# Performance work log

Measured on AMD Instinct MI355X. Metric: run time of the kernel, lower is better.

## Reference

```python
import jax, jax.numpy as jnp
import numpy as np

B, A, C = 64, 8732, 81


def setup_inputs() -> dict:
    key = jax.random.key(0)
    k1, k2, k3, k4, k5 = jax.random.split(key, 5)
    scores = jax.random.normal(k1, (B, A, C), dtype=jnp.float32)
    boxes = jax.random.normal(k2, (B, A, 4), dtype=jnp.float32)
    gt_labels = jax.random.randint(k3, (B, A), 0, C)
    gt_boxes = jax.random.normal(k4, (B, A, 4), dtype=jnp.float32)
    mask = jax.random.uniform(k5, (B, A)) < 0.02
    return {"scores": scores, "boxes": boxes, "gt_labels": gt_labels,
            "gt_boxes": gt_boxes, "mask": mask}


def reference(scores, boxes, gt_labels, gt_boxes, mask):
    dtype = scores.dtype
    maskf = mask.astype(dtype)
    pos_num = mask.sum(axis=-1, keepdims=True)          # [B,1] per-image positives
    N = jnp.maximum(1, mask.sum()).astype(dtype)        # max(1, total positives)

    # localization: smooth L1 (beta=1) summed over positive anchors
    d = boxes - gt_boxes
    ad = jnp.abs(d)
    sl1 = jnp.where(ad < 1.0, 0.5 * d * d, ad - 0.5)    # [B,A,4]
    loc_loss = (sl1.sum(axis=-1) * maskf).sum() / N

    # per-anchor cross entropy
    logp = jax.nn.log_softmax(scores, axis=-1)          # [B,A,C]
    c_loss = -jnp.take_along_axis(logp, gt_labels[..., None], axis=-1)[..., 0]  # [B,A]

    # hard negative mining: zero positives, rank by descending loss, keep top 3*pos_num
    conf_neg = jnp.where(mask, jnp.zeros((), dtype), c_loss)
    conf_idx = jnp.argsort(-conf_neg, axis=-1)          # descending sort indices
    rank = jnp.argsort(conf_idx, axis=-1)               # rank of each anchor
    neg_mask = rank < 3 * pos_num                       # [B,A]

    conf_loss = ((c_loss * maskf).sum() + (c_loss * neg_mask.astype(dtype)).sum()) / N
    total_loss = loc_loss + conf_loss
    return total_loss, loc_loss, conf_loss
```

## Files before the change

kernel.cpp:

```cpp
#include <hip/hip_runtime.h>
#include <hip/hip_bf16.h>
#include <math.h>

#define NB 64
#define NA 8732
#define NC 81
#define TOTAL (NB * NA)
#define APB 128
#define TPB 512
#define NBLK (TOTAL / APB)


__global__ void init_kernel(int* __restrict__ pos_count, float* __restrict__ acc) {
    const int t = threadIdx.x;
    if (t < NB) pos_count[t] = 0;
    else if (t < NB + 3) acc[t - NB] = 0.0f;
}

__device__ __forceinline__ float quadsum(float x) {
    x += __int_as_float(__builtin_amdgcn_update_dpp(
        0, __float_as_int(x), 0xB1, 0xF, 0xF, true));
    x += __int_as_float(__builtin_amdgcn_update_dpp(
        0, __float_as_int(x), 0x4E, 0xF, 0xF, true));
    return x;
}

__global__ __launch_bounds__(TPB) void main_kernel(
    const float* __restrict__ scores, const float* __restrict__ boxes,
    const int* __restrict__ gt_labels, const float* __restrict__ gt_boxes,
    const int* __restrict__ mask, float* __restrict__ conf_neg,
    int* __restrict__ pos_count, float* __restrict__ block_loc,
    float* __restrict__ block_pcs)
{
    __shared__ float lds[APB * NC];
    __shared__ float wredl[8], wredp[8];
    __shared__ int posc[2];
    const int tid  = threadIdx.x;
    const int lane = tid & 63;
    const int wid  = tid >> 6;
    const int base = blockIdx.x * APB;
    const int b0   = base / NA;

    if (tid < 2) posc[tid] = 0;
    __syncthreads();

    const float4* __restrict__ src = (const float4*)(scores + (size_t)base * NC);
    float4* dst = (float4*)lds;
    const float4 t0 = src[tid];
    const float4 t1 = src[tid + 512];
    const float4 t2 = src[tid + 1024];
    const float4 t3 = src[tid + 1536];
    const float4 t4 = src[tid + 2048];
    float4 t5;
    if (tid < 32) t5 = src[tid + 2560];
    dst[tid] = t0; dst[tid + 512] = t1; dst[tid + 1024] = t2;
    dst[tid + 1536] = t3; dst[tid + 2048] = t4;
    if (tid < 32) dst[tid + 2560] = t5;

    float loc = 0.0f;
    if (tid < APB) {
        const int a = base + tid;
        if (mask[a]) {
            const float4 bx = *(const float4*)(boxes    + (size_t)a * 4);
            const float4 gb = *(const float4*)(gt_boxes + (size_t)a * 4);
            const float d0 = bx.x - gb.x, d1 = bx.y - gb.y;
            const float d2 = bx.z - gb.z, d3 = bx.w - gb.w;
            const float a0 = fabsf(d0), a1 = fabsf(d1), a2 = fabsf(d2), a3 = fabsf(d3);
            loc = (a0 < 1.f ? 0.5f * d0 * d0 : a0 - 0.5f)
                + (a1 < 1.f ? 0.5f * d1 * d1 : a1 - 0.5f)
                + (a2 < 1.f ? 0.5f * d2 * d2 : a2 - 0.5f)
                + (a3 < 1.f ? 0.5f * d3 * d3 : a3 - 0.5f);
            atomicAdd(&posc[(a / NA) - b0], 1);
        }
    }
    __syncthreads();

    const int al = tid >> 2;
    const int q  = tid & 3;
    const float* __restrict__ row = lds + al * NC;
    float e = 0.0f;
    #pragma unroll
    for (int j = 0; j < 20; ++j) e += __expf(row[q * 20 + j]);
    if (q == 3) e += __expf(row[80]);
    e = quadsum(e);

    float pcs = 0.0f;
    if (q == 0) {
        const int a = base + al;
        const int lab = gt_labels[a];
        const float c = __logf(e) - row[lab];
        const int m = mask[a];
        conf_neg[a] = m ? 0.f : c;
        pcs = m ? c : 0.f;
    }

    #pragma unroll
    for (int o = 32; o; o >>= 1) {
        loc += __shfl_down(loc, o);
        pcs += __shfl_down(pcs, o);
    }
    if (lane == 0) { wredl[wid] = loc; wredp[wid] = pcs; }
    __syncthreads();
    if (tid == 0) {
        float sl = 0.f, sp = 0.f;
        #pragma unroll
        for (int w = 0; w < 8; ++w) { sl += wredl[w]; sp += wredp[w]; }
        block_loc[blockIdx.x] = sl;
        block_pcs[blockIdx.x] = sp;
    }
    if (tid < 2 && posc[tid] > 0)
        atomicAdd(&pos_count[b0 + tid], posc[tid]);
}

__global__ __launch_bounds__(1024) void topk_kernel(
    const float* __restrict__ conf_neg, const int* __restrict__ pos_count,
    float* __restrict__ acc)
{
    __shared__ unsigned sv[NA];
    __shared__ __align__(16) int whist[64][256];
    __shared__ int hist4[4][256];
    __shared__ int   redi[16];
    __shared__ float redf[16];
    __shared__ unsigned spfx;
    __shared__ int skr;
    const int tid  = threadIdx.x;
    const int lane = tid & 63;
    const int wid  = tid >> 6;
    const int hid  = tid >> 4;
    const int b = blockIdx.x;
    const float* __restrict__ row = conf_neg + (size_t)b * NA;

    int k = 3 * pos_count[b];
    if (k <= 0) return;
    if (k > NA) k = NA;

    for (int i = tid; i < NA; i += 1024) sv[i] = __float_as_uint(row[i]);
    __syncthreads();

    unsigned prefix = 0u;
    int kr = k;
    for (int shift = 24; shift >= 0; shift -= 8) {
        int4* w4 = (int4*)whist;
        const int4 z = make_int4(0, 0, 0, 0);
        w4[tid] = z; w4[tid + 1024] = z; w4[tid + 2048] = z; w4[tid + 3072] = z;
        __syncthreads();

        const unsigned himask = (shift == 24) ? 0u : (0xFFFFFFFFu << (shift + 8));
        for (int i = tid; i < NA; i += 1024) {
            const unsigned v = sv[i];
            if ((v & himask) == prefix)
                atomicAdd(&whist[hid][(v >> shift) & 255], 1);
        }
        __syncthreads();

        {
            const int p = tid >> 8;
            const int bb = tid & 255;
            int s = 0;
            #pragma unroll
            for (int w = 0; w < 16; ++w) s += whist[(p << 4) + w][bb];
            hist4[p][bb] = s;
        }
        __syncthreads();

        if (wid == 0) {
            int h0, h1, h2, h3;
            {
                const int b0i = 4 * lane;
                h0 = hist4[0][b0i]     + hist4[1][b0i]     + hist4[2][b0i]     + hist4[3][b0i];
                h1 = hist4[0][b0i + 1] + hist4[1][b0i + 1] + hist4[2][b0i + 1] + hist4[3][b0i + 1];
                h2 = hist4[0][b0i + 2] + hist4[1][b0i + 2] + hist4[2][b0i + 2] + hist4[3][b0i + 2];
                h3 = hist4[0][b0i + 3] + hist4[1][b0i + 3] + hist4[2][b0i + 3] + hist4[3][b0i + 3];
            }
            const int s3 = h3, s2 = h2 + s3, s1 = h1 + s2, s0 = h0 + s1;
            int incl = s0;
            #pragma unroll
            for (int off = 1; off < 64; off <<= 1) {
                const int v = __shfl_down(incl, off);
                if (lane + off < 64) incl += v;
            }
            const int E = incl - s0;
            const int S0 = E + s0, S1 = E + s1, S2 = E + s2, S3 = E + s3;
            if (S0 >= kr && S1 < kr) { spfx = prefix | ((unsigned)(4 * lane)     << shift); skr = kr - S1; }
            else if (S1 >= kr && S2 < kr) { spfx = prefix | ((unsigned)(4 * lane + 1) << shift); skr = kr - S2; }
            else if (S2 >= kr && S3 < kr) { spfx = prefix | ((unsigned)(4 * lane + 2) << shift); skr = kr - S3; }
            else if (S3 >= kr && E  < kr) { spfx = prefix | ((unsigned)(4 * lane + 3) << shift); skr = kr - E;  }
        }
        __syncthreads();
        prefix = spfx;
        kr = skr;
    }

    float s = 0.0f; int cg = 0;
    for (int i = tid; i < NA; i += 1024) {
        const unsigned u = sv[i];
        if (u > prefix) { s += __uint_as_float(u); cg++; }
    }
    #pragma unroll
    for (int o = 32; o; o >>= 1) { s += __shfl_down(s, o); cg += __shfl_down(cg, o); }
    if ((tid & 63) == 0) { redf[wid] = s; redi[wid] = cg; }
    __syncthreads();
    if (tid == 0) {
        float ts = 0.f; int tc = 0;
        #pragma unroll
        for (int w = 0; w < 16; ++w) { ts += redf[w]; tc += redi[w]; }
        ts += (float)(k - tc) * __uint_as_float(prefix);
        atomicAdd(&acc[2], ts);
    }
}

__global__ __launch_bounds__(1024) void final_kernel(
    const float* __restrict__ block_loc, const float* __restrict__ block_pcs,
    const int* __restrict__ pos_count, const float* __restrict__ acc,
    float* __restrict__ out)
{
    __shared__ float rl[16], rp[16];
    const int tid = threadIdx.x;
    const int wid = tid >> 6;
    float sl = 0.f, sp = 0.f;
    for (int i = tid; i < NBLK; i += 1024) { sl += block_loc[i]; sp += block_pcs[i]; }
    int p = (tid < NB) ? pos_count[tid] : 0;
    #pragma unroll
    for (int o = 32; o; o >>= 1) {
        sl += __shfl_down(sl, o);
        sp += __shfl_down(sp, o);
        p  += __shfl_down(p, o);
    }
    if ((tid & 63) == 0) { rl[wid] = sl; rp[wid] = sp; }
    __syncthreads();
    if (tid == 0) {
        float tl = 0.f, tp = 0.f;
        #pragma unroll
        for (int w = 0; w < 16; ++w) { tl += rl[w]; tp += rp[w]; }
        const float N = fmaxf(1.0f, (float)p);
        const float loc  = tl / N;
        const float conf = (tp + acc[2]) / N;
        out[0] = loc + conf;
        out[1] = loc;
        out[2] = conf;
    }
}

extern "C" void kernel_launch(void* const* d_in, const int* in_sizes, int n_in,
                              void* d_out, int out_size, void* d_ws, size_t ws_size,
                              hipStream_t stream) {
    const float* scores    = (const float*)d_in[0];
    const float* boxes     = (const float*)d_in[1];
    const int*   gt_labels = (const int*)d_in[2];
    const float* gt_boxes  = (const float*)d_in[3];
    const int*   mask      = (const int*)d_in[4];
    float* out = (float*)d_out;

    float* conf_neg  = (float*)d_ws;
    int*   pos_count = (int*)(conf_neg + TOTAL);
    float* acc       = (float*)(pos_count + NB);
    float* block_loc = acc + 3;
    float* block_pcs = block_loc + NBLK;

    hipLaunchKernelGGL(init_kernel, dim3(1), dim3(128), 0, stream, pos_count, acc);
    hipLaunchKernelGGL(main_kernel, dim3(NBLK), dim3(TPB), 0, stream,
                       scores, boxes, gt_labels, gt_boxes, mask,
                       conf_neg, pos_count, block_loc, block_pcs);
    hipLaunchKernelGGL(topk_kernel, dim3(NB), dim3(1024), 0, stream,
                       conf_neg, pos_count, acc);
    hipLaunchKernelGGL(final_kernel, dim3(1), dim3(1024), 0, stream,
                       block_loc, block_pcs, pos_count, acc, out);
}
```

Measured before the change: 292.1 us.

## Use direct global-to-LDS loads and drop init kernel via per-image counts

The score tile is now loaded with global_load_lds, which writes straight into shared memory instead of staging through registers. Per-image positive counting moves from shared and global atomics in the main kernel into the top-k kernel, which re-reads the mask row. The top-k kernel now writes a per-image partial sum instead of an atomic accumulate, so the init kernel and its launch can be removed. The trade-off is an extra mask read per image in the top-k kernel, and it relies on the direct-to-LDS load path behaving correctly here.

```diff
diff --git a/kernel.cpp b/kernel.cpp
--- a/kernel.cpp
+++ b/kernel.cpp
@@ -1,5 +1,4 @@
 #include <hip/hip_runtime.h>
-#include <hip/hip_bf16.h>
 #include <math.h>
 
 #define NB 64
@@ -11,12 +10,6 @@
 #define NBLK (TOTAL / APB)
 
 
-__global__ void init_kernel(int* __restrict__ pos_count, float* __restrict__ acc) {
-    const int t = threadIdx.x;
-    if (t < NB) pos_count[t] = 0;
-    else if (t < NB + 3) acc[t - NB] = 0.0f;
-}
-
 __device__ __forceinline__ float quadsum(float x) {
     x += __int_as_float(__builtin_amdgcn_update_dpp(
         0, __float_as_int(x), 0xB1, 0xF, 0xF, true));
@@ -25,37 +18,34 @@
     return x;
 }
 
+__device__ __forceinline__ void gload_lds16(const float4* g, float4* l) {
+    __builtin_amdgcn_global_load_lds(
+        (const __attribute__((address_space(1))) unsigned int*)g,
+        (__attribute__((address_space(3))) unsigned int*)l,
+        16, 0, 0);
+}
+
 __global__ __launch_bounds__(TPB) void main_kernel(
     const float* __restrict__ scores, const float* __restrict__ boxes,
     const int* __restrict__ gt_labels, const float* __restrict__ gt_boxes,
     const int* __restrict__ mask, float* __restrict__ conf_neg,
-    int* __restrict__ pos_count, float* __restrict__ block_loc,
-    float* __restrict__ block_pcs)
+    float* __restrict__ block_loc, float* __restrict__ block_pcs)
 {
     __shared__ float lds[APB * NC];
     __shared__ float wredl[8], wredp[8];
-    __shared__ int posc[2];
     const int tid  = threadIdx.x;
     const int lane = tid & 63;
     const int wid  = tid >> 6;
     const int base = blockIdx.x * APB;
-    const int b0   = base / NA;
-
-    if (tid < 2) posc[tid] = 0;
-    __syncthreads();
 
     const float4* __restrict__ src = (const float4*)(scores + (size_t)base * NC);
     float4* dst = (float4*)lds;
-    const float4 t0 = src[tid];
-    const float4 t1 = src[tid + 512];
-    const float4 t2 = src[tid + 1024];
-    const float4 t3 = src[tid + 1536];
-    const float4 t4 = src[tid + 2048];
-    float4 t5;
-    if (tid < 32) t5 = src[tid + 2560];
-    dst[tid] = t0; dst[tid + 512] = t1; dst[tid + 1024] = t2;
-    dst[tid + 1536] = t3; dst[tid + 2048] = t4;
-    if (tid < 32) dst[tid + 2560] = t5;
+    gload_lds16(src + tid,        dst + tid);
+    gload_lds16(src + tid +  512, dst + tid +  512);
+    gload_lds16(src + tid + 1024, dst + tid + 1024);
+    gload_lds16(src + tid + 1536, dst + tid + 1536);
+    gload_lds16(src + tid + 2048, dst + tid + 2048);
+    if (tid < 32) gload_lds16(src + tid + 2560, dst + tid + 2560);
 
     float loc = 0.0f;
     if (tid < APB) {
@@ -70,7 +60,6 @@
                 + (a1 < 1.f ? 0.5f * d1 * d1 : a1 - 0.5f)
                 + (a2 < 1.f ? 0.5f * d2 * d2 : a2 - 0.5f)
                 + (a3 < 1.f ? 0.5f * d3 * d3 : a3 - 0.5f);
-            atomicAdd(&posc[(a / NA) - b0], 1);
         }
     }
     __syncthreads();
@@ -108,13 +97,11 @@
         block_loc[blockIdx.x] = sl;
         block_pcs[blockIdx.x] = sp;
     }
-    if (tid < 2 && posc[tid] > 0)
-        atomicAdd(&pos_count[b0 + tid], posc[tid]);
 }
 
 __global__ __launch_bounds__(1024) void topk_kernel(
-    const float* __restrict__ conf_neg, const int* __restrict__ pos_count,
-    float* __restrict__ acc)
+    const float* __restrict__ conf_neg, const int* __restrict__ mask,
+    int* __restrict__ pos_count, float* __restrict__ accv)
 {
     __shared__ unsigned sv[NA];
     __shared__ __align__(16) int whist[64][256];
@@ -123,19 +110,39 @@
     __shared__ float redf[16];
     __shared__ unsigned spfx;
     __shared__ int skr;
+    __shared__ int sk;
     const int tid  = threadIdx.x;
     const int lane = tid & 63;
     const int wid  = tid >> 6;
     const int hid  = tid >> 4;
     const int b = blockIdx.x;
-    const float* __restrict__ row = conf_neg + (size_t)b * NA;
-
-    int k = 3 * pos_count[b];
-    if (k <= 0) return;
-    if (k > NA) k = NA;
-
-    for (int i = tid; i < NA; i += 1024) sv[i] = __float_as_uint(row[i]);
-    __syncthreads();
+    const float* __restrict__ row  = conf_neg + (size_t)b * NA;
+    const int*   __restrict__ mrow = mask     + (size_t)b * NA;
+
+    int myc = 0;
+    for (int i = tid; i < NA; i += 1024) {
+        sv[i] = __float_as_uint(row[i]);
+        myc += mrow[i];
+    }
+    #pragma unroll
+    for (int o = 32; o; o >>= 1) myc += __shfl_down(myc, o);
+    if (lane == 0) redi[wid] = myc;
+    __syncthreads();
+    if (tid == 0) {
+        int p = 0;
+        #pragma unroll
+        for (int w = 0; w < 16; ++w) p += redi[w];
+        pos_count[b] = p;
+        int kk = 3 * p;
+        if (kk > NA) kk = NA;
+        sk = kk;
+    }
+    __syncthreads();
+    int k = sk;
+    if (k <= 0) {
+        if (tid == 0) accv[b] = 0.0f;
+        return;
+    }
 
     unsigned prefix = 0u;
     int kr = k;
@@ -205,13 +212,13 @@
         #pragma unroll
         for (int w = 0; w < 16; ++w) { ts += redf[w]; tc += redi[w]; }
         ts += (float)(k - tc) * __uint_as_float(prefix);
-        atomicAdd(&acc[2], ts);
+        accv[b] = ts;
     }
 }
 
 __global__ __launch_bounds__(1024) void final_kernel(
     const float* __restrict__ block_loc, const float* __restrict__ block_pcs,
-    const int* __restrict__ pos_count, const float* __restrict__ acc,
+    const int* __restrict__ pos_count, const float* __restrict__ accv,
     float* __restrict__ out)
 {
     __shared__ float rl[16], rp[16];
@@ -219,12 +226,14 @@
     const int wid = tid >> 6;
     float sl = 0.f, sp = 0.f;
     for (int i = tid; i < NBLK; i += 1024) { sl += block_loc[i]; sp += block_pcs[i]; }
-    int p = (tid < NB) ? pos_count[tid] : 0;
+    int   p  = (tid < NB) ? pos_count[tid] : 0;
+    float sa = (tid < NB) ? accv[tid]      : 0.f;
     #pragma unroll
     for (int o = 32; o; o >>= 1) {
         sl += __shfl_down(sl, o);
         sp += __shfl_down(sp, o);
         p  += __shfl_down(p, o);
+        sa += __shfl_down(sa, o);
     }
     if ((tid & 63) == 0) { rl[wid] = sl; rp[wid] = sp; }
     __syncthreads();
@@ -234,7 +243,7 @@
         for (int w = 0; w < 16; ++w) { tl += rl[w]; tp += rp[w]; }
         const float N = fmaxf(1.0f, (float)p);
         const float loc  = tl / N;
-        const float conf = (tp + acc[2]) / N;
+        const float conf = (tp + sa) / N;
         out[0] = loc + conf;
         out[1] = loc;
         out[2] = conf;
@@ -253,16 +262,15 @@
 
     float* conf_neg  = (float*)d_ws;
     int*   pos_count = (int*)(conf_neg + TOTAL);
-    float* acc       = (float*)(pos_count + NB);
-    float* block_loc = acc + 3;
+    float* accv      = (float*)(pos_count + NB);
+    float* block_loc = accv + NB;
     float* block_pcs = block_loc + NBLK;
 
-    hipLaunchKernelGGL(init_kernel, dim3(1), dim3(128), 0, stream, pos_count, acc);
     hipLaunchKernelGGL(main_kernel, dim3(NBLK), dim3(TPB), 0, stream,
                        scores, boxes, gt_labels, gt_boxes, mask,
-                       conf_neg, pos_count, block_loc, block_pcs);
+                       conf_neg, block_loc, block_pcs);
     hipLaunchKernelGGL(topk_kernel, dim3(NB), dim3(1024), 0, stream,
-                       conf_neg, pos_count, acc);
+                       conf_neg, mask, pos_count, accv);
     hipLaunchKernelGGL(final_kernel, dim3(1), dim3(1024), 0, stream,
-                       block_loc, block_pcs, pos_count, acc, out);
-}
+                       block_loc, block_pcs, pos_count, accv, out);
+}
```

Result: faster. 284.0 us, median of 2 (-2.8%).
